# Kernel tuning notes

Hardware: AMD Instinct MI355X
Metric: run time of the kernel (lower is better)

Reference implementation:

```python
import jax, jax.numpy as jnp
import numpy as np
import math

G = 256      # graphs per batch
N0 = 256     # nodes per graph at input
RATIO = 0.5  # TopKPooling ratio


def gcn_conv(x, src, dst, ew, W, b):
    h = x @ W
    n = x.shape[0]
    deg = jnp.zeros((n,), x.dtype).at[dst].add(ew) + 1.0  # +1 for self-loop
    dinv = jax.lax.rsqrt(deg)
    norm = dinv[src] * dinv[dst] * ew
    agg = jnp.zeros_like(h).at[dst].add(norm[:, None] * h[src])
    return agg + h / deg[:, None] + b  # self-loop norm = 1/deg


def topk_pool(x, src, dst, ew, w, n_per_graph):
    # PyG TopKPooling: score = tanh(x.w/||w||); keep top ceil(ratio*n) per graph;
    # x_out = x[perm] * score[perm]; edges between dropped nodes are masked out.
    k = int(math.ceil(RATIO * n_per_graph))
    score = jnp.tanh((x @ w) / jnp.linalg.norm(w))
    top_s, top_i = jax.lax.top_k(score.reshape(G, n_per_graph), k)  # [G,k]
    perm = (top_i + (jnp.arange(G) * n_per_graph)[:, None]).reshape(-1)
    new_x = x[perm] * top_s.reshape(-1, 1)
    new_id = jnp.full((x.shape[0],), -1, jnp.int32).at[perm].set(
        jnp.arange(G * k, dtype=jnp.int32))
    ns, nd = new_id[src], new_id[dst]
    valid = (ns >= 0) & (nd >= 0)
    new_ew = ew * valid.astype(x.dtype)
    ns = jnp.where(valid, ns, 0)
    nd = jnp.where(valid, nd, 0)
    new_batch = jnp.repeat(jnp.arange(G, dtype=jnp.int32), k)
    return new_x, ns, nd, new_ew, new_batch, k


def readout(x, batch):
    # torch.cat([global_max_pool, global_mean_pool], dim=1)
    mx = jax.ops.segment_max(x, batch, num_segments=G)
    cnt = jax.ops.segment_sum(jnp.ones((x.shape[0],), x.dtype), batch, num_segments=G)
    mn = jax.ops.segment_sum(x, batch, num_segments=G) / cnt[:, None]
    return jnp.concatenate([mx, mn], axis=1)


def _forward(x, edge_index, batch, gcn_w0, gcn_b0, gcn_w1, gcn_b1, gcn_w2, gcn_b2,
             pool_w0, pool_w1, pool_w2, lin1_w, lin1_b, lin2_w, lin2_b, lin3_w, lin3_b):
    src, dst = edge_index[0], edge_index[1]
    ew = jnp.ones((src.shape[0],), x.dtype)
    npg = N0
    h = jax.nn.relu(gcn_conv(x, src, dst, ew, gcn_w0, gcn_b0))
    h, src, dst, ew, batch, npg = topk_pool(h, src, dst, ew, pool_w0, npg)
    out = readout(h, batch)
    for Wg, bg, pw in ((gcn_w1, gcn_b1, pool_w1), (gcn_w2, gcn_b2, pool_w2)):
        h = jax.nn.relu(gcn_conv(h, src, dst, ew, Wg, bg))
        h, src, dst, ew, batch, npg = topk_pool(h, src, dst, ew, pw, npg)
        out = out + readout(h, batch)
    h1 = jax.nn.relu(out @ lin1_w + lin1_b)  # dropout = identity (eval mode)
    h2 = jax.nn.relu(h1 @ lin2_w + lin2_b)
    logits = h2 @ lin3_w + lin3_b
    return jax.nn.log_softmax(logits, axis=-1)


def setup_inputs() -> dict:
    key = jax.random.key(0)
    ks = jax.random.split(key, 16)
    EPG = 2048  # edges per graph (avg degree 8)
    F_IN, H = 128, 256
    num_nodes, E = G * N0, G * EPG
    x = jax.random.normal(ks[0], (num_nodes, F_IN), jnp.float32)
    offs = jnp.repeat(jnp.arange(G, dtype=jnp.int32) * N0, EPG)
    src = offs + jax.random.randint(ks[1], (E,), 0, N0, dtype=jnp.int32)
    dst = offs + jax.random.randint(ks[2], (E,), 0, N0, dtype=jnp.int32)

    def glorot(k, shape):
        lim = float(np.sqrt(6.0 / (shape[0] + shape[1])))
        return jax.random.uniform(k, shape, jnp.float32, -lim, lim)

    return {
        "x": x,
        "edge_index": jnp.stack([src, dst]),
        "batch": jnp.arange(num_nodes, dtype=jnp.int32) // N0,
        "gcn_w0": glorot(ks[3], (F_IN, H)), "gcn_b0": jnp.zeros((H,), jnp.float32),
        "gcn_w1": glorot(ks[4], (H, H)), "gcn_b1": jnp.zeros((H,), jnp.float32),
        "gcn_w2": glorot(ks[5], (H, H)), "gcn_b2": jnp.zeros((H,), jnp.float32),
        "pool_w0": jax.random.normal(ks[6], (H,), jnp.float32) * 0.1,
        "pool_w1": jax.random.normal(ks[7], (H,), jnp.float32) * 0.1,
        "pool_w2": jax.random.normal(ks[8], (H,), jnp.float32) * 0.1,
        "lin1_w": glorot(ks[9], (2 * H, H)), "lin1_b": jnp.zeros((H,), jnp.float32),
        "lin2_w": glorot(ks[10], (H, H // 2)), "lin2_b": jnp.zeros((H // 2,), jnp.float32),
        "lin3_w": glorot(ks[11], (H // 2, 2)), "lin3_b": jnp.zeros((2,), jnp.float32),
    }


def reference(x, edge_index, batch, gcn_w0, gcn_b0, gcn_w1, gcn_b1, gcn_w2, gcn_b2,
              pool_w0, pool_w1, pool_w2, lin1_w, lin1_b, lin2_w, lin2_b, lin3_w, lin3_b):
    return _forward(x, edge_index, batch, gcn_w0, gcn_b0, gcn_w1, gcn_b1, gcn_w2, gcn_b2,
                    pool_w0, pool_w1, pool_w2, lin1_w, lin1_b, lin2_w, lin2_b, lin3_w, lin3_b)
```

## Files before the change

### kernel.cpp

```cpp
#include <hip/hip_runtime.h>
#include <hip/hip_bf16.h>
#include <math.h>

#define G_GRAPHS 256
#define EPG 2048
#define E_TOT 524288
#define HF 256
#define FIN 128

template <int K>
__global__ __launch_bounds__(256, 4)
void gemm_v8(const float* __restrict__ A, const float* __restrict__ W,
             float* __restrict__ C) {
    __shared__ __align__(16) float As[32 * 68];
    __shared__ __align__(16) float Wa[32 * 68];
    __shared__ __align__(16) float Wb[32 * 68];
    const int tid = threadIdx.x;
    const int tx = tid & 15;
    const int ty = tid >> 4;
    const int r0 = blockIdx.x * 64;
    const int c0 = blockIdx.y * 128;
    const int l8 = tid >> 3;
    const int kq = tid & 7;
    const int wkk = tid >> 5;
    const int wc = tid & 31;
    float acc[4][8] = {{0.f}};
    float4 va0, va1, vw0, vw1, vw2, vw3;

    auto load_regs = [&](int k0) {
        va0 = *(const float4*)&A[(size_t)(r0 + l8) * K + k0 + 4 * kq];
        va1 = *(const float4*)&A[(size_t)(r0 + 32 + l8) * K + k0 + 4 * kq];
        vw0 = *(const float4*)&W[(size_t)(k0 + 0  + wkk) * 256 + c0 + 4 * wc];
        vw1 = *(const float4*)&W[(size_t)(k0 + 8  + wkk) * 256 + c0 + 4 * wc];
        vw2 = *(const float4*)&W[(size_t)(k0 + 16 + wkk) * 256 + c0 + 4 * wc];
        vw3 = *(const float4*)&W[(size_t)(k0 + 24 + wkk) * 256 + c0 + 4 * wc];
    };
    auto write_stage = [&]() {
        {
            int rs = l8 ^ (kq << 3);
            As[(4 * kq + 0) * 68 + rs] = va0.x;
            As[(4 * kq + 1) * 68 + rs] = va0.y;
            As[(4 * kq + 2) * 68 + rs] = va0.z;
            As[(4 * kq + 3) * 68 + rs] = va0.w;
        }
        {
            int rs = (32 + l8) ^ (kq << 3);
            As[(4 * kq + 0) * 68 + rs] = va1.x;
            As[(4 * kq + 1) * 68 + rs] = va1.y;
            As[(4 * kq + 2) * 68 + rs] = va1.z;
            As[(4 * kq + 3) * 68 + rs] = va1.w;
        }
        if (wc < 16) {
            *(float4*)&Wa[(0  + wkk) * 68 + 4 * wc] = vw0;
            *(float4*)&Wa[(8  + wkk) * 68 + 4 * wc] = vw1;
            *(float4*)&Wa[(16 + wkk) * 68 + 4 * wc] = vw2;
            *(float4*)&Wa[(24 + wkk) * 68 + 4 * wc] = vw3;
        } else {
            *(float4*)&Wb[(0  + wkk) * 68 + 4 * (wc - 16)] = vw0;
            *(float4*)&Wb[(8  + wkk) * 68 + 4 * (wc - 16)] = vw1;
            *(float4*)&Wb[(16 + wkk) * 68 + 4 * (wc - 16)] = vw2;
            *(float4*)&Wb[(24 + wkk) * 68 + 4 * (wc - 16)] = vw3;
        }
    };
    auto compute = [&]() {
#pragma unroll 4
        for (int kk = 0; kk < 32; ++kk) {
            const int g = (ty * 4) ^ ((kk >> 2) << 3);
            const float4 a0 = *(const float4*)&As[kk * 68 + g];
            const float4 w0 = *(const float4*)&Wa[kk * 68 + tx * 4];
            const float4 w1 = *(const float4*)&Wb[kk * 68 + tx * 4];
            float av[4] = {a0.x, a0.y, a0.z, a0.w};
            float wv_[8] = {w0.x, w0.y, w0.z, w0.w, w1.x, w1.y, w1.z, w1.w};
#pragma unroll
            for (int i = 0; i < 4; ++i)
#pragma unroll
                for (int j = 0; j < 8; ++j)
                    acc[i][j] += av[i] * wv_[j];
        }
    };

    load_regs(0);
    write_stage();
    __syncthreads();
    for (int k0 = 0; k0 < K - 32; k0 += 32) {
        load_regs(k0 + 32);
        compute();
        __syncthreads();
        write_stage();
        __syncthreads();
    }
    compute();

#pragma unroll
    for (int i = 0; i < 4; ++i) {
        float4 v0 = make_float4(acc[i][0], acc[i][1], acc[i][2], acc[i][3]);
        float4 v1 = make_float4(acc[i][4], acc[i][5], acc[i][6], acc[i][7]);
        size_t base = (size_t)(r0 + ty * 4 + i) * 256 + c0 + tx * 4;
        *(float4*)&C[base] = v0;
        *(float4*)&C[base + 64] = v1;
    }
}

template <bool IDENT>
__device__ __forceinline__ void csr_body(
    const int* __restrict__ ei, int g, int t, int npg, const int* curL,
    int* __restrict__ degS, float* __restrict__ dinvS,
    int* __restrict__ startsS, int2* __restrict__ slots2,
    int* cul, short* dstv, unsigned char* rnk, int (*h)[256],
    int* cnt, int* st) {
    const int lane = t & 63;
    const int wv = t >> 6;
    for (int i = t; i < 32 * 256; i += 256) ((int*)h)[i] = 0;
    for (int e = t; e < EPG; e += 256) {
        size_t idx = (size_t)g * EPG + e;
        int u = ei[idx] - g * 256;
        int v = ei[E_TOT + idx] - g * 256;
        int cu = IDENT ? u : curL[u];
        int cv = IDENT ? v : curL[v];
        bool valid = (cu >= 0 && cv >= 0);
        cul[e] = cu;
        dstv[e] = valid ? (short)cv : (short)256;
    }
    __syncthreads();
    for (int c = wv; c < 32; c += 4) {
        int e = c * 64 + lane;
        int d = (int)dstv[e];
        unsigned long long m = ~0ULL;
#pragma unroll
        for (int b = 0; b < 9; ++b) {
            unsigned long long bb = __ballot((d >> b) & 1);
            m &= ((d >> b) & 1) ? bb : ~bb;
        }
        int r = __popcll(m & ((1ULL << lane) - 1ULL));
        rnk[e] = (unsigned char)r;
        if (r == 0 && d < 256) h[c][d] = __popcll(m);
    }
    __syncthreads();
    if (t < npg) {
        int run = 0;
        for (int c = 0; c < 32; ++c) { int v = h[c][t]; h[c][t] = run; run += v; }
        cnt[t] = run;
        degS[g * npg + t] = run + 1;
        dinvS[g * npg + t] = 1.0f / sqrtf((float)(run + 1));
    }
    __syncthreads();
    if (t == 0) {
        int run = 0;
        for (int i = 0; i < npg; ++i) { st[i] = run; run += cnt[i]; }
    }
    __syncthreads();
    if (t < npg) startsS[g * npg + t] = g * EPG + st[t];
    for (int e = t; e < EPG; e += 256) {
        int d = (int)dstv[e];
        if (d < npg) {
            int slot = st[d] + h[e >> 6][d] + (int)rnk[e];
            int cu = cul[e];
            float dv = 1.0f / sqrtf((float)(cnt[cu] + 1));
            slots2[g * EPG + slot] = make_int2(g * npg + cu, __float_as_int(dv));
        }
    }
}

__global__ __launch_bounds__(256)
void fused_init_csr(const int* __restrict__ ei, int* __restrict__ cur,
                    int* __restrict__ degS, float* __restrict__ dinvS,
                    int* __restrict__ startsS, int2* __restrict__ slots2) {
    __shared__ int cul[EPG];
    __shared__ short dstv[EPG];
    __shared__ unsigned char rnk[EPG];
    __shared__ int h[32][256];
    __shared__ int cnt[256];
    __shared__ int st[256];
    const int g = blockIdx.x;
    const int t = threadIdx.x;
    cur[g * 256 + t] = t;
    csr_body<true>(ei, g, t, 256, nullptr, degS, dinvS, startsS, slots2,
                   cul, dstv, rnk, h, cnt, st);
}

__global__ __launch_bounds__(256)
void agg_score2(const int* __restrict__ degS, const float* __restrict__ dinvS,
                const int* __restrict__ startsS, const int2* __restrict__ slots2,
                const float* __restrict__ HL, float* __restrict__ H2,
                const float* __restrict__ bias, const float* __restrict__ pw,
                float* __restrict__ score, int nbOver8) {
    __shared__ float vrow[4][256];
    const int t = threadIdx.x;
    const int wv = t >> 6;
    const int lane = t & 63;
    const int blk = (blockIdx.x & 7) * nbOver8 + (blockIdx.x >> 3);
    const int node = blk * 4 + wv;
    const int cntE = degS[node] - 1;
    const float degF = (float)(cntE + 1);
    const float dn = dinvS[node];
    const int2* sl = slots2 + startsS[node];
    float ax = 0.f, ay = 0.f, az = 0.f, aw = 0.f;
    int j = 0;
    for (; j + 8 <= cntE; j += 8) {
        int2 s[8];
#pragma unroll
        for (int u = 0; u < 8; ++u) s[u] = sl[j + u];
        float4 hv[8];
#pragma unroll
        for (int u = 0; u < 8; ++u)
            hv[u] = *(const float4*)&HL[(size_t)s[u].x * 256 + 4 * lane];
#pragma unroll
        for (int u = 0; u < 8; ++u) {
            float dv = __int_as_float(s[u].y);
            ax += dv * hv[u].x; ay += dv * hv[u].y;
            az += dv * hv[u].z; aw += dv * hv[u].w;
        }
    }
    for (; j + 4 <= cntE; j += 4) {
        int2 s[4];
#pragma unroll
        for (int u = 0; u < 4; ++u) s[u] = sl[j + u];
        float4 hv[4];
#pragma unroll
        for (int u = 0; u < 4; ++u)
            hv[u] = *(const float4*)&HL[(size_t)s[u].x * 256 + 4 * lane];
#pragma unroll
        for (int u = 0; u < 4; ++u) {
            float dv = __int_as_float(s[u].y);
            ax += dv * hv[u].x; ay += dv * hv[u].y;
            az += dv * hv[u].z; aw += dv * hv[u].w;
        }
    }
    for (; j < cntE; ++j) {
        int2 sv = sl[j];
        float dv = __int_as_float(sv.y);
        float4 hv = *(const float4*)&HL[(size_t)sv.x * 256 + 4 * lane];
        ax += dv * hv.x; ay += dv * hv.y; az += dv * hv.z; aw += dv * hv.w;
    }
    const float4 hn = *(const float4*)&HL[(size_t)node * 256 + 4 * lane];
    const float4 bi = *(const float4*)&bias[4 * lane];
    float4 v;
    v.x = ax * dn + hn.x / degF + bi.x;  v.x = fmaxf(v.x, 0.f);
    v.y = ay * dn + hn.y / degF + bi.y;  v.y = fmaxf(v.y, 0.f);
    v.z = az * dn + hn.z / degF + bi.z;  v.z = fmaxf(v.z, 0.f);
    v.w = aw * dn + hn.w / degF + bi.w;  v.w = fmaxf(v.w, 0.f);
    *(float4*)&H2[(size_t)node * 256 + 4 * lane] = v;
    *(float4*)&vrow[wv][4 * lane] = v;
    float pr = 0.f, s2p = 0.f;
    for (int jj = 0; jj < 4; ++jj) {
        int f = lane + 64 * jj;
        float w = pw[f];
        pr += vrow[wv][f] * w;
        s2p += w * w;
    }
    for (int off = 32; off; off >>= 1) {
        pr += __shfl_down(pr, off, 64);
        s2p += __shfl_down(s2p, off, 64);
    }
    s2p = __shfl(s2p, 0, 64);
    if (lane == 0) score[node] = tanhf(pr / sqrtf(s2p));
}

__global__ __launch_bounds__(256)
void fused_topk_csr(const float* __restrict__ score, int npg, int k,
                    const float* __restrict__ H2, float* __restrict__ OUT,
                    float* __restrict__ outacc, int* __restrict__ cur, int first,
                    const int* __restrict__ ei,
                    int* __restrict__ degS, float* __restrict__ dinvS,
                    int* __restrict__ startsS, int2* __restrict__ slots2) {
    __shared__ float ss[256];
    __shared__ int si_[256];
    __shared__ int rankOf[256];
    __shared__ int curL[256];
    __shared__ int cul[EPG];
    __shared__ short dstv[EPG];
    __shared__ unsigned char rnk[EPG];
    __shared__ int h[32][256];
    __shared__ int cnt[256];
    __shared__ int st[256];
    const int g = blockIdx.x;
    const int t = threadIdx.x;
    if (t < npg) { ss[t] = score[g * npg + t]; si_[t] = t; }
    else         { ss[t] = -INFINITY; si_[t] = 0x7FFFFFFF; }
    for (int size = 2; size <= 256; size <<= 1) {
        for (int stride = size >> 1; stride > 0; stride >>= 1) {
            __syncthreads();
            int i = t, j = t ^ stride;
            if (j > i) {
                float a = ss[i], b = ss[j];
                int ia = si_[i], ib = si_[j];
                bool inOrder = (a > b) || (a == b && ia < ib);
                bool desc = ((i & size) == 0);
                if (desc ? !inOrder : inOrder) {
                    ss[i] = b; ss[j] = a; si_[i] = ib; si_[j] = ia;
                }
            }
        }
    }
    __syncthreads();
    rankOf[t] = -1;
    __syncthreads();
    if (t < k) rankOf[si_[t]] = t;
    __syncthreads();
    {
        int v = g * 256 + t;
        int c = cur[v];
        int nc = (c >= 0) ? rankOf[c] : -1;
        cur[v] = nc;
        curL[t] = nc;
    }
    const size_t gb = (size_t)g * npg * 256;
    float mx = -INFINITY, sm = 0.f;
    for (int n = 0; n < k; n += 4) {
        float v0 = H2[gb + (size_t)si_[n + 0] * 256 + t] * ss[n + 0];
        float v1 = H2[gb + (size_t)si_[n + 1] * 256 + t] * ss[n + 1];
        float v2 = H2[gb + (size_t)si_[n + 2] * 256 + t] * ss[n + 2];
        float v3 = H2[gb + (size_t)si_[n + 3] * 256 + t] * ss[n + 3];
        size_t ob = ((size_t)g * k + n) * 256 + t;
        OUT[ob]       = v0;
        OUT[ob + 256] = v1;
        OUT[ob + 512] = v2;
        OUT[ob + 768] = v3;
        mx = fmaxf(mx, v0); sm += v0;
        mx = fmaxf(mx, v1); sm += v1;
        mx = fmaxf(mx, v2); sm += v2;
        mx = fmaxf(mx, v3); sm += v3;
    }
    float mean = sm / (float)k;
    if (first) {
        outacc[g * 512 + t] = mx;
        outacc[g * 512 + 256 + t] = mean;
    } else {
        outacc[g * 512 + t] += mx;
        outacc[g * 512 + 256 + t] += mean;
    }
    __syncthreads();
    csr_body<false>(ei, g, t, k, curL, degS, dinvS, startsS, slots2,
                    cul, dstv, rnk, h, cnt, st);
}

__global__ __launch_bounds__(256)
void fused_topk_mlp(const float* __restrict__ score, int npg, int k,
                    const float* __restrict__ H2,
                    const float* __restrict__ outacc,
                    const float* __restrict__ l1w, const float* __restrict__ l1b,
                    const float* __restrict__ l2w, const float* __restrict__ l2b,
                    const float* __restrict__ l3w, const float* __restrict__ l3b,
                    float* __restrict__ out) {
    __shared__ float ss[256];
    __shared__ int si_[256];
    __shared__ float row[512];
    __shared__ float h1[256];
    __shared__ float h2[128];
    const int g = blockIdx.x;
    const int t = threadIdx.x;
    if (t < npg) { ss[t] = score[g * npg + t]; si_[t] = t; }
    else         { ss[t] = -INFINITY; si_[t] = 0x7FFFFFFF; }
    for (int size = 2; size <= 256; size <<= 1) {
        for (int stride = size >> 1; stride > 0; stride >>= 1) {
            __syncthreads();
            int i = t, j = t ^ stride;
            if (j > i) {
                float a = ss[i], b = ss[j];
                int ia = si_[i], ib = si_[j];
                bool inOrder = (a > b) || (a == b && ia < ib);
                bool desc = ((i & size) == 0);
                if (desc ? !inOrder : inOrder) {
                    ss[i] = b; ss[j] = a; si_[i] = ib; si_[j] = ia;
                }
            }
        }
    }
    __syncthreads();
    const size_t gb = (size_t)g * npg * 256;
    float mx = -INFINITY, sm = 0.f;
    for (int n = 0; n < k; n += 4) {
        float v0 = H2[gb + (size_t)si_[n + 0] * 256 + t] * ss[n + 0];
        float v1 = H2[gb + (size_t)si_[n + 1] * 256 + t] * ss[n + 1];
        float v2 = H2[gb + (size_t)si_[n + 2] * 256 + t] * ss[n + 2];
        float v3 = H2[gb + (size_t)si_[n + 3] * 256 + t] * ss[n + 3];
        mx = fmaxf(mx, v0); sm += v0;
        mx = fmaxf(mx, v1); sm += v1;
        mx = fmaxf(mx, v2); sm += v2;
        mx = fmaxf(mx, v3); sm += v3;
    }
    float mean = sm / (float)k;
    row[t]       = outacc[g * 512 + t] + mx;
    row[256 + t] = outacc[g * 512 + 256 + t] + mean;
    __syncthreads();
    {
        float a = l1b[t];
        for (int j = 0; j < 512; ++j) a += row[j] * l1w[j * 256 + t];
        h1[t] = fmaxf(a, 0.f);
    }
    __syncthreads();
    if (t < 128) {
        float a2 = l2b[t];
        for (int j = 0; j < 256; ++j) a2 += h1[j] * l2w[j * 128 + t];
        h2[t] = fmaxf(a2, 0.f);
    }
    __syncthreads();
    if (t == 0) {
        float l0 = l3b[0], l1 = l3b[1];
        for (int j = 0; j < 128; ++j) {
            float h = h2[j];
            l0 += h * l3w[j * 2 + 0];
            l1 += h * l3w[j * 2 + 1];
        }
        float m = fmaxf(l0, l1);
        float lse = m + logf(expf(l0 - m) + expf(l1 - m));
        out[g * 2 + 0] = l0 - lse;
        out[g * 2 + 1] = l1 - lse;
    }
}

__global__ __launch_bounds__(256, 1)
void gnn_mono(const float* __restrict__ x, const int* __restrict__ ei,
              const float* __restrict__ gw0, const float* __restrict__ gb0,
              const float* __restrict__ gw1, const float* __restrict__ gb1,
              const float* __restrict__ gw2, const float* __restrict__ gb2,
              const float* __restrict__ pw0, const float* __restrict__ pw1,
              const float* __restrict__ pw2,
              const float* __restrict__ l1w, const float* __restrict__ l1b,
              const float* __restrict__ l2w, const float* __restrict__ l2b,
              const float* __restrict__ l3w, const float* __restrict__ l3b,
              float* __restrict__ out, float* __restrict__ ws) {
    const int g = blockIdx.x;
    const int t = threadIdx.x;
    float* P = ws + (size_t)g * HF * 256;
    float* Q = ws + (size_t)G_GRAPHS * HF * 256 + (size_t)g * HF * 256;
    __shared__ int   eb[EPG];
    __shared__ int   slots[EPG];
    __shared__ int   curID[256];
    __shared__ int   cntL[256];
    __shared__ int   startL[256];
    __shared__ float degF[256];
    __shared__ float dinv[256];
    __shared__ float sa[256];
    __shared__ float ss[256];
    __shared__ int   si_[256];
    __shared__ float scoreV[256];
    __shared__ int   kept[128];
    __shared__ int   rankOf[256];
    __shared__ float row[512];
    for (int e = t; e < EPG; e += 256) {
        size_t idx = (size_t)g * EPG + e;
        eb[e] = ((ei[idx] - g * 256) << 8) | (ei[E_TOT + idx] - g * 256);
    }
    curID[t] = t;
    float accMx = 0.f, accMn = 0.f;
    const float* GW[3] = {gw0, gw1, gw2};
    const float* GB[3] = {gb0, gb1, gb2};
    const float* PW[3] = {pw0, pw1, pw2};
    const int kk[3] = {128, 64, 32};
    int npg = 256;
    __syncthreads();
    for (int s = 0; s < 3; ++s) {
        const int knext = kk[s];
        {
            const float* Wp = GW[s];
            const int K = (s == 0) ? FIN : HF;
            for (int n = 0; n < npg; ++n) {
                if (s == 0) { if (t < FIN) sa[t] = x[(size_t)(g * 256 + n) * FIN + t]; }
                else sa[t] = P[(size_t)n * HF + t];
                __syncthreads();
                float a = 0.f;
                for (int k2 = 0; k2 < K; ++k2) a += sa[k2] * Wp[k2 * HF + t];
                Q[(size_t)n * HF + t] = a;
                __syncthreads();
            }
        }
        cntL[t] = 0;
        __syncthreads();
        for (int e = t; e < EPG; e += 256) {
            int p = eb[e];
            int cu = curID[p >> 8], cv = curID[p & 255];
            if (cu >= 0 && cv >= 0) atomicAdd(&cntL[cv], 1);
        }
        __syncthreads();
        if (t == 0) { int run = 0; for (int i = 0; i < npg; ++i) { startL[i] = run; run += cntL[i]; } }
        __syncthreads();
        if (t < npg) {
            float d = (float)cntL[t] + 1.0f;
            degF[t] = d;
            dinv[t] = 1.0f / sqrtf(d);
            int c = startL[t];
            for (int e = 0; e < EPG; ++e) {
                int p = eb[e];
                int cu = curID[p >> 8], cv = curID[p & 255];
                if (cu >= 0 && cv >= 0 && cv == t) slots[c++] = e;
            }
        }
        __syncthreads();
        {
            const float bb = GB[s][t];
            for (int n = 0; n < npg; ++n) {
                float acc = 0.f;
                const int s0 = startL[n], s1 = s0 + cntL[n];
                for (int j = s0; j < s1; ++j) {
                    int scur = curID[eb[slots[j]] >> 8];
                    acc += dinv[scur] * Q[(size_t)scur * HF + t];
                }
                float v = acc * dinv[n] + Q[(size_t)n * HF + t] / degF[n] + bb;
                P[(size_t)n * HF + t] = fmaxf(v, 0.f);
            }
        }
        __syncthreads();
        {
            const float* pwp = PW[s];
            const int lane = t & 63, wv = t >> 6;
            float s2p = 0.f;
            for (int j = 0; j < 4; ++j) { float w = pwp[lane + 64 * j]; s2p += w * w; }
            for (int off = 32; off; off >>= 1) s2p += __shfl_down(s2p, off, 64);
            s2p = __shfl(s2p, 0, 64);
            const float nw = sqrtf(s2p);
            for (int n = wv; n < npg; n += 4) {
                float pr = 0.f;
                for (int j = 0; j < 4; ++j) { int f = lane + 64 * j; pr += P[(size_t)n * HF + f] * pwp[f]; }
                for (int off = 32; off; off >>= 1) pr += __shfl_down(pr, off, 64);
                if (lane == 0) scoreV[n] = tanhf(pr / nw);
            }
        }
        __syncthreads();
        if (t < npg) { ss[t] = scoreV[t]; si_[t] = t; }
        else         { ss[t] = -INFINITY; si_[t] = 0x7FFFFFFF; }
        for (int size = 2; size <= 256; size <<= 1) {
            for (int stride = size >> 1; stride > 0; stride >>= 1) {
                __syncthreads();
                int i = t, j = t ^ stride;
                if (j > i) {
                    float a = ss[i], b = ss[j];
                    int ia = si_[i], ib = si_[j];
                    bool inOrder = (a > b) || (a == b && ia < ib);
                    bool desc = ((i & size) == 0);
                    if (desc ? !inOrder : inOrder) { ss[i] = b; ss[j] = a; si_[i] = ib; si_[j] = ia; }
                }
            }
        }
        __syncthreads();
        if (t < knext) kept[t] = si_[t];
        __syncthreads();
        {
            float mx = -INFINITY, sm = 0.f;
            for (int n = 0; n < knext; ++n) {
                int o = kept[n];
                float vv = P[(size_t)o * HF + t] * scoreV[o];
                Q[(size_t)n * HF + t] = vv;
                mx = fmaxf(mx, vv);
                sm += vv;
            }
            accMx += mx;
            accMn += sm / (float)knext;
        }
        rankOf[t] = -1;
        __syncthreads();
        if (t < knext) rankOf[kept[t]] = t;
        __syncthreads();
        { int c = curID[t]; curID[t] = (c >= 0) ? rankOf[c] : -1; }
        __syncthreads();
        { float* tmp = P; P = Q; Q = tmp; }
        npg = knext;
    }
    row[t] = accMx;
    row[256 + t] = accMn;
    __syncthreads();
    { float a = l1b[t]; for (int j = 0; j < 512; ++j) a += row[j] * l1w[j * 256 + t]; scoreV[t] = fmaxf(a, 0.f); }
    __syncthreads();
    if (t < 128) { float a2 = l2b[t]; for (int j = 0; j < 256; ++j) a2 += scoreV[j] * l2w[j * 128 + t]; sa[t] = fmaxf(a2, 0.f); }
    __syncthreads();
    if (t == 0) {
        float l0 = l3b[0], l1 = l3b[1];
        for (int j = 0; j < 128; ++j) { float h = sa[j]; l0 += h * l3w[j * 2 + 0]; l1 += h * l3w[j * 2 + 1]; }
        float m = fmaxf(l0, l1);
        float lse = m + logf(expf(l0 - m) + expf(l1 - m));
        out[g * 2 + 0] = l0 - lse;
        out[g * 2 + 1] = l1 - lse;
    }
}

extern "C" void kernel_launch(void* const* d_in, const int* in_sizes, int n_in,
                              void* d_out, int out_size, void* d_ws, size_t ws_size,
                              hipStream_t stream) {
    const float* x   = (const float*)d_in[0];
    const int*   ei  = (const int*)d_in[1];
    const float* gw0 = (const float*)d_in[3];
    const float* gb0 = (const float*)d_in[4];
    const float* gw1 = (const float*)d_in[5];
    const float* gb1 = (const float*)d_in[6];
    const float* gw2 = (const float*)d_in[7];
    const float* gb2 = (const float*)d_in[8];
    const float* pw0 = (const float*)d_in[9];
    const float* pw1 = (const float*)d_in[10];
    const float* pw2 = (const float*)d_in[11];
    const float* l1w = (const float*)d_in[12];
    const float* l1b = (const float*)d_in[13];
    const float* l2w = (const float*)d_in[14];
    const float* l2b = (const float*)d_in[15];
    const float* l3w = (const float*)d_in[16];
    const float* l3b = (const float*)d_in[17];
    float* out = (float*)d_out;

    const size_t SLAB = (size_t)65536 * 256;
    char* p = (char*)d_ws;
    float* P      = (float*)p; p += SLAB * 4;
    float* Q      = (float*)p; p += SLAB * 4;
    int*   cur    = (int*)p;   p += (size_t)65536 * 4;
    int*   degS   = (int*)p;   p += (size_t)65536 * 4;
    float* dinvS  = (float*)p; p += (size_t)65536 * 4;
    int*   starts = (int*)p;   p += (size_t)65536 * 4;
    int2*  slots2 = (int2*)p;  p += (size_t)E_TOT * 8;
    float* score  = (float*)p; p += (size_t)65536 * 4;
    int*   kept   = (int*)p;   p += (size_t)32768 * 4;
    float* outacc = (float*)p; p += (size_t)G_GRAPHS * 512 * 4;
    const size_t needed = (size_t)(p - (char*)d_ws);

    if (ws_size < needed) {
        gnn_mono<<<G_GRAPHS, 256, 0, stream>>>(
            x, ei, gw0, gb0, gw1, gb1, gw2, gb2, pw0, pw1, pw2,
            l1w, l1b, l2w, l2b, l3w, l3b, out, (float*)d_ws);
        return;
    }

    const int   npg[3] = {256, 128, 64};
    const int   kk[3]  = {128, 64, 32};
    const int   Ns[3]  = {65536, 32768, 16384};
    const float* GW[3] = {gw0, gw1, gw2};
    const float* GB[3] = {gb0, gb1, gb2};
    const float* PW[3] = {pw0, pw1, pw2};

    float* HLs[3]   = {P, Q, P};
    float* H2s[3]   = {Q, P, Q};
    float* POOLs[3] = {P, Q, P};

    fused_init_csr<<<G_GRAPHS, 256, 0, stream>>>(ei, cur, degS, dinvS,
                                                 starts, slots2);

    for (int s = 0; s < 3; ++s) {
        const int n = Ns[s];
        const int k = kk[s];
        if (s == 0) {
            gemm_v8<FIN><<<dim3(n / 64, 2), 256, 0, stream>>>(x, GW[s], HLs[s]);
        } else {
            gemm_v8<HF><<<dim3(n / 64, 2), 256, 0, stream>>>(POOLs[s - 1], GW[s], HLs[s]);
        }
        agg_score2<<<n / 4, 256, 0, stream>>>(degS, dinvS, starts, slots2,
                                              HLs[s], H2s[s], GB[s], PW[s], score,
                                              n / 32);
        if (s < 2) {
            fused_topk_csr<<<G_GRAPHS, 256, 0, stream>>>(
                score, npg[s], k, H2s[s], POOLs[s], outacc, cur, s == 0 ? 1 : 0,
                ei, degS, dinvS, starts, slots2);
        } else {
            fused_topk_mlp<<<G_GRAPHS, 256, 0, stream>>>(
                score, npg[s], k, H2s[s], outacc,
                l1w, l1b, l2w, l2b, l3w, l3b, out);
        }
    }
}
```

Before: 444.0 us.

## Add 128x128-tile FP32 GEMM with 8x8 per-thread outputs for first two stages

Adds a new GEMM kernel with 128-row by 128-column block tiles, 8x8 register tiles per thread and a K-step of 16. Shared memory for A is stored transposed with an XOR swizzle to avoid bank conflicts. Stages 0 and 1 use the new kernel, and stage 2 keeps the old 64-row kernel. The larger tiles raise arithmetic intensity per shared-memory load, at the cost of more registers, fewer blocks and possibly lower occupancy.

```diff
diff --git a/kernel.cpp b/kernel.cpp
--- a/kernel.cpp
+++ b/kernel.cpp
@@ -7,6 +7,7 @@
 #define E_TOT 524288
 #define HF 256
 #define FIN 128
+
 
 template <int K>
 __global__ __launch_bounds__(256, 4)
@@ -96,6 +97,95 @@
         float4 v0 = make_float4(acc[i][0], acc[i][1], acc[i][2], acc[i][3]);
         float4 v1 = make_float4(acc[i][4], acc[i][5], acc[i][6], acc[i][7]);
         size_t base = (size_t)(r0 + ty * 4 + i) * 256 + c0 + tx * 4;
+        *(float4*)&C[base] = v0;
+        *(float4*)&C[base + 64] = v1;
+    }
+}
+
+template <int K>
+__global__ __launch_bounds__(256, 4)
+void gemm_v12(const float* __restrict__ A, const float* __restrict__ W,
+              float* __restrict__ C) {
+    __shared__ __align__(16) float As[16 * 132];
+    __shared__ __align__(16) float Wa[16 * 68];
+    __shared__ __align__(16) float Wb[16 * 68];
+    const int tid = threadIdx.x;
+    const int tx = tid & 15;
+    const int ty = tid >> 4;
+    const int r0 = blockIdx.x * 128;
+    const int c0 = blockIdx.y * 128;
+    const int sr = tid >> 1;
+    const int sq = tid & 1;
+    const int wkk = tid >> 5;
+    const int wc = tid & 31;
+    float acc[8][8] = {{0.f}};
+    float4 va0, va1, vw0, vw1;
+
+    auto load_regs = [&](int k0) {
+        va0 = *(const float4*)&A[(size_t)(r0 + sr) * K + k0 + 4 * sq];
+        va1 = *(const float4*)&A[(size_t)(r0 + sr) * K + k0 + 8 + 4 * sq];
+        vw0 = *(const float4*)&W[(size_t)(k0 + wkk) * 256 + c0 + 4 * wc];
+        vw1 = *(const float4*)&W[(size_t)(k0 + 8 + wkk) * 256 + c0 + 4 * wc];
+    };
+    auto write_stage = [&]() {
+        {
+            int rs = sr ^ (sq << 3);
+            As[(4 * sq + 0) * 132 + rs] = va0.x;
+            As[(4 * sq + 1) * 132 + rs] = va0.y;
+            As[(4 * sq + 2) * 132 + rs] = va0.z;
+            As[(4 * sq + 3) * 132 + rs] = va0.w;
+        }
+        {
+            int kq = sq + 2;
+            int rs = sr ^ (kq << 3);
+            As[(4 * kq + 0) * 132 + rs] = va1.x;
+            As[(4 * kq + 1) * 132 + rs] = va1.y;
+            As[(4 * kq + 2) * 132 + rs] = va1.z;
+            As[(4 * kq + 3) * 132 + rs] = va1.w;
+        }
+        if (wc < 16) {
+            *(float4*)&Wa[wkk * 68 + 4 * wc] = vw0;
+            *(float4*)&Wa[(8 + wkk) * 68 + 4 * wc] = vw1;
+        } else {
+            *(float4*)&Wb[wkk * 68 + 4 * (wc - 16)] = vw0;
+            *(float4*)&Wb[(8 + wkk) * 68 + 4 * (wc - 16)] = vw1;
+        }
+    };
+    auto compute = [&]() {
+#pragma unroll 4
+        for (int kk = 0; kk < 16; ++kk) {
+            const int g = (ty ^ (kk >> 2)) << 3;
+            const float4 a0 = *(const float4*)&As[kk * 132 + g];
+            const float4 a1 = *(const float4*)&As[kk * 132 + g + 4];
+            const float4 w0 = *(const float4*)&Wa[kk * 68 + tx * 4];
+            const float4 w1 = *(const float4*)&Wb[kk * 68 + tx * 4];
+            float av[8] = {a0.x, a0.y, a0.z, a0.w, a1.x, a1.y, a1.z, a1.w};
+            float wv_[8] = {w0.x, w0.y, w0.z, w0.w, w1.x, w1.y, w1.z, w1.w};
+#pragma unroll
+            for (int i = 0; i < 8; ++i)
+#pragma unroll
+                for (int j = 0; j < 8; ++j)
+                    acc[i][j] += av[i] * wv_[j];
+        }
+    };
+
+    load_regs(0);
+    write_stage();
+    __syncthreads();
+    for (int k0 = 0; k0 < K - 16; k0 += 16) {
+        load_regs(k0 + 16);
+        compute();
+        __syncthreads();
+        write_stage();
+        __syncthreads();
+    }
+    compute();
+
+#pragma unroll
+    for (int i = 0; i < 8; ++i) {
+        float4 v0 = make_float4(acc[i][0], acc[i][1], acc[i][2], acc[i][3]);
+        float4 v1 = make_float4(acc[i][4], acc[i][5], acc[i][6], acc[i][7]);
+        size_t base = (size_t)(r0 + ty * 8 + i) * 256 + c0 + tx * 4;
         *(float4*)&C[base] = v0;
         *(float4*)&C[base + 64] = v1;
     }
@@ -634,7 +724,9 @@
         const int n = Ns[s];
         const int k = kk[s];
         if (s == 0) {
-            gemm_v8<FIN><<<dim3(n / 64, 2), 256, 0, stream>>>(x, GW[s], HLs[s]);
+            gemm_v12<FIN><<<dim3(n / 128, 2), 256, 0, stream>>>(x, GW[s], HLs[s]);
+        } else if (s == 1) {
+            gemm_v12<HF><<<dim3(n / 128, 2), 256, 0, stream>>>(POOLs[s - 1], GW[s], HLs[s]);
         } else {
             gemm_v8<HF><<<dim3(n / 64, 2), 256, 0, stream>>>(POOLs[s - 1], GW[s], HLs[s]);
         }
```

Result: faster. 421.2 us (-5.1%).
